# Optimization experiments

Hardware: AMD Instinct MI355X
Metric: run time of the kernel (lower is better)

Reference implementation:

```python
import jax, jax.numpy as jnp
import numpy as np

N = 2_097_152
TABLE = 32768  # hash table size (power of 2 -> mod == & 32767)
FEAT = 16
H = 64


def setup_inputs() -> dict:
    key = jax.random.key(0)
    k = jax.random.split(key, 9)
    pos = jax.random.normal(k[0], (N, 3), dtype=jnp.float32)
    normal = jax.random.normal(k[1], (N, 3), dtype=jnp.float32)
    emb = jax.random.normal(k[2], (TABLE, FEAT), dtype=jnp.float32) * 0.05
    W1 = jax.random.normal(k[3], (FEAT + 3, H), dtype=jnp.float32) * 0.1
    b1 = jnp.zeros((H,), jnp.float32)
    W2 = jax.random.normal(k[4], (H, H), dtype=jnp.float32) * 0.1
    b2 = jnp.zeros((H,), jnp.float32)
    W3 = jax.random.normal(k[5], (H, 3), dtype=jnp.float32) * 0.1
    b3 = jnp.zeros((3,), jnp.float32)
    return {"pos": pos, "normal": normal, "emb": emb,
            "W1": W1, "b1": b1, "W2": W2, "b2": b2, "W3": W3, "b3": b3}


def _hash_idx(pos):
    # torch .long() truncates toward zero; astype(int32) does the same.
    # Products only matter mod 2^15, so int32 wraparound is safe.
    s = (pos * 8.0).astype(jnp.int32)
    h = (s[:, 0] * np.int32(73856093)) ^ (s[:, 1] * np.int32(19349663)) ^ (s[:, 2] * np.int32(83492791))
    return h & np.int32(TABLE - 1)  # floor-mod by 2^15 == bitwise AND


def reference(pos, normal, emb, W1, b1, W2, b2, W3, b3):
    idx = _hash_idx(pos)                    # [N] int32
    feat = emb[idx]                         # [N,16] gather
    x = jnp.concatenate([feat, normal], axis=-1)  # [N,19]
    h1 = jax.nn.relu(x @ W1 + b1)           # [N,64]
    h2 = jax.nn.relu(h1 @ W2 + b2)          # [N,64]
    return jax.nn.sigmoid(h2 @ W3 + b3)     # [N,3]
```

## Files before the change

kernel.cpp:

```cpp
#include <hip/hip_runtime.h>
#include <cstdint>


typedef short  bf16x8 __attribute__((ext_vector_type(8)));
typedef float  f32x4  __attribute__((ext_vector_type(4)));

#define MFMA16(A, B, C) __builtin_amdgcn_mfma_f32_16x16x32_bf16((A), (B), (C), 0, 0, 0)

__device__ inline int pk(float a, float b) {
    int d;
    __asm__("v_cvt_pk_bf16_f32 %0, %1, %2" : "=v"(d) : "v"(a), "v"(b));
    return d;
}
__device__ inline uint32_t f2b_u(float f) {
    union { float f; uint32_t u; } x; x.f = f;
    return (x.u + 0x7FFFu + ((x.u >> 16) & 1u)) >> 16;
}
__device__ inline short f2b(float f) { return (short)f2b_u(f); }

__device__ inline void pl32_swap(int& a, int& b) {
    __asm__ volatile("v_permlane32_swap_b32 %0, %1" : "+v"(a), "+v"(b));
}
__device__ inline void pl16_swap(int& a, int& b) {
    __asm__ volatile("v_permlane16_swap_b32 %0, %1" : "+v"(a), "+v"(b));
}

__device__ inline void cfence() { __asm__ volatile("" ::: "memory"); }

__device__ inline float sigmoid_fast(float x) {
    float e = __expf(-x);
    return __builtin_amdgcn_rcpf(1.0f + e);
}

__device__ inline void cd_to_frag(const f32x4 acc[4], int4& lo, int4& hi) {
    int P0 = pk(fmaxf(acc[0][0],0.f), fmaxf(acc[0][1],0.f));
    int P1 = pk(fmaxf(acc[0][2],0.f), fmaxf(acc[0][3],0.f));
    int P2 = pk(fmaxf(acc[1][0],0.f), fmaxf(acc[1][1],0.f));
    int P3 = pk(fmaxf(acc[1][2],0.f), fmaxf(acc[1][3],0.f));
    int P4 = pk(fmaxf(acc[2][0],0.f), fmaxf(acc[2][1],0.f));
    int P5 = pk(fmaxf(acc[2][2],0.f), fmaxf(acc[2][3],0.f));
    int P6 = pk(fmaxf(acc[3][0],0.f), fmaxf(acc[3][1],0.f));
    int P7 = pk(fmaxf(acc[3][2],0.f), fmaxf(acc[3][3],0.f));
    pl32_swap(P0, P2); pl16_swap(P0, P2);
    pl32_swap(P1, P3); pl16_swap(P1, P3);
    pl32_swap(P4, P6); pl16_swap(P4, P6);
    pl32_swap(P5, P7); pl16_swap(P5, P7);
    lo = make_int4(P0, P1, P2, P3);
    hi = make_int4(P4, P5, P6, P7);
}

__device__ inline bf16x8 as_frag(int4 v) {
    bf16x8 f; __builtin_memcpy(&f, &v, sizeof(f)); return f;
}

#define XS 40

__global__ __launch_bounds__(256, 4) void nrad_mfma_kernel(
    const float* __restrict__ pos, const float* __restrict__ nrm,
    const float* __restrict__ emb,
    const float* __restrict__ W1, const float* __restrict__ b1,
    const float* __restrict__ W2, const float* __restrict__ b2,
    const float* __restrict__ W3, const float* __restrict__ b3,
    float* __restrict__ out, int ntiles)
{
    __shared__ alignas(16) char arena[20480];
    short* w1t = (short*)arena;
    short* w2t = (short*)(arena + 4096);
    short* w3t = (short*)(arena + 12288);
    float* b2s = (float*)(arena + 12672);
    float* b3s = (float*)(arena + 12928);

    const int tid  = threadIdx.x;
    const int wave = tid >> 6;
    const int lane = tid & 63;
    const int q    = lane >> 4;
    const int nn   = lane & 15;

    for (int e = tid; e < 64 * 32; e += 256) {
        int n = e >> 5, k = e & 31;
        float v = (k < 19) ? W1[k * 64 + n] : (k == 19 ? b1[n] : 0.0f);
        w1t[n * 32 + k] = f2b(v);
    }
    for (int e = tid; e < 4096; e += 256) {
        int k = e >> 6, n = e & 63;
        w2t[n * 64 + k] = f2b(W2[e]);
    }
    for (int e = tid; e < 192; e += 256) {
        int k = e / 3, c = e - k * 3;
        w3t[c * 64 + k] = f2b(W3[e]);
    }
    for (int e = tid; e < 64; e += 256) b2s[e] = b2[e];
    if (tid < 4) b3s[tid] = (tid < 3) ? b3[tid] : 0.0f;
    __syncthreads();

    bf16x8 w1f[4], w2f[4][2], w3f[2];
    #pragma unroll
    for (int t = 0; t < 4; ++t)
        w1f[t] = *(const bf16x8*)(w1t + (t * 16 + nn) * 32 + q * 8);
    #pragma unroll
    for (int t = 0; t < 4; ++t)
        #pragma unroll
        for (int ks = 0; ks < 2; ++ks)
            w2f[t][ks] = *(const bf16x8*)(w2t + (t * 16 + nn) * 64 + ks * 32 + q * 8);
    {
        int c3 = (nn < 3) ? nn : 0;
        w3f[0] = *(const bf16x8*)(w3t + c3 * 64 + q * 8);
        w3f[1] = *(const bf16x8*)(w3t + c3 * 64 + 32 + q * 8);
    }
    f32x4 b2rv[4];
    #pragma unroll
    for (int t = 0; t < 4; ++t)
        b2rv[t] = *(const f32x4*)(b2s + t * 16 + q * 4);
    const float b3r = (nn < 3) ? b3s[nn] : 0.0f;
    __syncthreads();

    short* xw = (short*)(arena + wave * 5120);

    const int xro  = nn * XS + q * 8;
    const int oofs = q * 12 + nn;

    const int wave_gid = blockIdx.x * 4 + wave;
    const int nwaves   = gridDim.x * 4;
    const float4* emb4 = (const float4*)emb;

    for (int tile = wave_gid; tile < ntiles; tile += nwaves) {
        const int base = tile * 64;
        const int i    = base + lane;

        const float* pp = pos + 3 * i;
        const float* np = nrm + 3 * i;
        float p0 = pp[0], p1 = pp[1], p2 = pp[2];
        float n0 = np[0], n1 = np[1], n2 = np[2];
        int s0 = (int)(p0 * 8.0f), s1 = (int)(p1 * 8.0f), s2 = (int)(p2 * 8.0f);
        uint32_t h = ((uint32_t)s0 * 73856093u) ^ ((uint32_t)s1 * 19349663u) ^
                     ((uint32_t)s2 * 83492791u);
        uint32_t idx = h & 32767u;
        float4 f0 = emb4[idx*4+0], f1 = emb4[idx*4+1];
        float4 f2 = emb4[idx*4+2], f3 = emb4[idx*4+3];

        int4 A = make_int4(pk(f0.x, f0.y), pk(f0.z, f0.w), pk(f1.x, f1.y), pk(f1.z, f1.w));
        int4 B = make_int4(pk(f2.x, f2.y), pk(f2.z, f2.w), pk(f3.x, f3.y), pk(f3.z, f3.w));
        int4 C = make_int4(pk(n0, n1), pk(n2, 1.0f), 0, 0);
        int4 D = make_int4(0, 0, 0, 0);
        int4* xr = (int4*)(xw + lane * XS);
        xr[0] = A; xr[1] = B; xr[2] = C; xr[3] = D;
        cfence();

        const float* ob = out + (size_t)base * 3;

        #pragma unroll
        for (int sub = 0; sub < 4; ++sub) {
            bf16x8 xf = *(const bf16x8*)(xw + sub * 16 * XS + xro);
            f32x4 acc1[4];
            #pragma unroll
            for (int t = 0; t < 4; ++t) {
                f32x4 z = {0.0f, 0.0f, 0.0f, 0.0f};
                acc1[t] = MFMA16(w1f[t], xf, z);
            }

            int4 h1lo, h1hi;
            cd_to_frag(acc1, h1lo, h1hi);
            bf16x8 h1f0 = as_frag(h1lo), h1f1 = as_frag(h1hi);

            f32x4 acc2[4];
            #pragma unroll
            for (int t = 0; t < 4; ++t) {
                f32x4 c2 = MFMA16(w2f[t][0], h1f0, b2rv[t]);
                acc2[t]  = MFMA16(w2f[t][1], h1f1, c2);
            }

            int4 h2lo, h2hi;
            cd_to_frag(acc2, h2lo, h2hi);
            bf16x8 h2f0 = as_frag(h2lo), h2f1 = as_frag(h2hi);

            f32x4 cb = {b3r, b3r, b3r, b3r};
            f32x4 c3a = MFMA16(h2f0, w3f[0], cb);
            f32x4 acc3 = MFMA16(h2f1, w3f[1], c3a);

            float o0 = sigmoid_fast(acc3[0]);
            float o1 = sigmoid_fast(acc3[1]);
            float o2 = sigmoid_fast(acc3[2]);
            float o3 = sigmoid_fast(acc3[3]);
            if (nn < 3) {
                float* o = (float*)(ob + sub * 48 + oofs);
                o[0] = o0; o[3] = o1; o[6] = o2; o[9] = o3;
            }
        }
        cfence();
    }
}

extern "C" void kernel_launch(void* const* d_in, const int* in_sizes, int n_in,
                              void* d_out, int out_size, void* d_ws, size_t ws_size,
                              hipStream_t stream) {
    const float* pos = (const float*)d_in[0];
    const float* nrm = (const float*)d_in[1];
    const float* emb = (const float*)d_in[2];
    const float* W1  = (const float*)d_in[3];
    const float* b1  = (const float*)d_in[4];
    const float* W2  = (const float*)d_in[5];
    const float* b2  = (const float*)d_in[6];
    const float* W3  = (const float*)d_in[7];
    const float* b3  = (const float*)d_in[8];
    float* out = (float*)d_out;

    int n = in_sizes[0] / 3;
    int ntiles = n / 64;
    int grid = 2048;
    nrad_mfma_kernel<<<grid, 256, 0, stream>>>(pos, nrm, emb, W1, b1, W2, b2,
                                               W3, b3, out, ntiles);
}
```

Before: 156.1 us.

## Prepack MLP weights in a setup kernel and interleave two MFMA sub-tiles

```diff
diff --git a/kernel.cpp b/kernel.cpp
--- a/kernel.cpp
+++ b/kernel.cpp
@@ -12,11 +12,6 @@
     __asm__("v_cvt_pk_bf16_f32 %0, %1, %2" : "=v"(d) : "v"(a), "v"(b));
     return d;
 }
-__device__ inline uint32_t f2b_u(float f) {
-    union { float f; uint32_t u; } x; x.f = f;
-    return (x.u + 0x7FFFu + ((x.u >> 16) & 1u)) >> 16;
-}
-__device__ inline short f2b(float f) { return (short)f2b_u(f); }
 
 __device__ inline void pl32_swap(int& a, int& b) {
     __asm__ volatile("v_permlane32_swap_b32 %0, %1" : "+v"(a), "+v"(b));
@@ -55,20 +50,68 @@
 
 #define XS 40
 
-__global__ __launch_bounds__(256, 4) void nrad_mfma_kernel(
+__global__ __launch_bounds__(256) void nrad_setup_kernel(
+    const float* __restrict__ W1, const float* __restrict__ b1,
+    const float* __restrict__ W2, const float* __restrict__ W3,
+    float* __restrict__ ws)
+{
+    const int tid  = threadIdx.x;
+    const int wv   = tid >> 6;
+    const int lane = tid & 63;
+    const int q    = lane >> 4;
+    const int nn   = lane & 15;
+    int4* w1o = (int4*)ws;
+    int4* w2o = (int4*)ws + 256;
+    int4* w3o = (int4*)ws + 768;
+
+    if (wv == 0) {
+        for (int t = 0; t < 4; ++t) {
+            int n = t * 16 + nn;
+            float v[8];
+            #pragma unroll
+            for (int j = 0; j < 8; ++j) {
+                int k = q * 8 + j;
+                v[j] = (k < 19) ? W1[k * 64 + n] : (k == 19 ? b1[n] : 0.0f);
+            }
+            w1o[t * 64 + lane] = make_int4(pk(v[0],v[1]), pk(v[2],v[3]),
+                                           pk(v[4],v[5]), pk(v[6],v[7]));
+        }
+    } else if (wv == 3) {
+        for (int h = 0; h < 2; ++h) {
+            float v[8];
+            #pragma unroll
+            for (int j = 0; j < 8; ++j) {
+                int k = h * 32 + q * 8 + j;
+                v[j] = (nn < 3) ? W3[k * 3 + nn] : 0.0f;
+            }
+            w3o[h * 64 + lane] = make_int4(pk(v[0],v[1]), pk(v[2],v[3]),
+                                           pk(v[4],v[5]), pk(v[6],v[7]));
+        }
+    } else {
+        for (int tt = 0; tt < 2; ++tt) {
+            int t = (wv - 1) * 2 + tt;
+            int n = t * 16 + nn;
+            for (int ks = 0; ks < 2; ++ks) {
+                float v[8];
+                #pragma unroll
+                for (int j = 0; j < 8; ++j) {
+                    int k = ks * 32 + q * 8 + j;
+                    v[j] = W2[k * 64 + n];
+                }
+                w2o[(t * 2 + ks) * 64 + lane] = make_int4(pk(v[0],v[1]), pk(v[2],v[3]),
+                                                          pk(v[4],v[5]), pk(v[6],v[7]));
+            }
+        }
+    }
+}
+
+__global__ __launch_bounds__(256, 3) void nrad_mfma_kernel(
     const float* __restrict__ pos, const float* __restrict__ nrm,
     const float* __restrict__ emb,
-    const float* __restrict__ W1, const float* __restrict__ b1,
-    const float* __restrict__ W2, const float* __restrict__ b2,
-    const float* __restrict__ W3, const float* __restrict__ b3,
-    float* __restrict__ out, int ntiles)
+    const float* __restrict__ b2, const float* __restrict__ b3,
+    const float* __restrict__ ws, float* __restrict__ out, int ntiles)
 {
-    __shared__ alignas(16) char arena[20480];
-    short* w1t = (short*)arena;
-    short* w2t = (short*)(arena + 4096);
-    short* w3t = (short*)(arena + 12288);
-    float* b2s = (float*)(arena + 12672);
-    float* b3s = (float*)(arena + 12928);
+    __shared__ alignas(16) short xbuf[4][64 * XS];
 
     const int tid  = threadIdx.x;
     const int wave = tid >> 6;
@@ -76,46 +119,23 @@
     const int q    = lane >> 4;
     const int nn   = lane & 15;
 
-    for (int e = tid; e < 64 * 32; e += 256) {
-        int n = e >> 5, k = e & 31;
-        float v = (k < 19) ? W1[k * 64 + n] : (k == 19 ? b1[n] : 0.0f);
-        w1t[n * 32 + k] = f2b(v);
-    }
-    for (int e = tid; e < 4096; e += 256) {
-        int k = e >> 6, n = e & 63;
-        w2t[n * 64 + k] = f2b(W2[e]);
-    }
-    for (int e = tid; e < 192; e += 256) {
-        int k = e / 3, c = e - k * 3;
-        w3t[c * 64 + k] = f2b(W3[e]);
-    }
-    for (int e = tid; e < 64; e += 256) b2s[e] = b2[e];
-    if (tid < 4) b3s[tid] = (tid < 3) ? b3[tid] : 0.0f;
-    __syncthreads();
-
+    const int4* wsf = (const int4*)ws;
     bf16x8 w1f[4], w2f[4][2], w3f[2];
     #pragma unroll
-    for (int t = 0; t < 4; ++t)
-        w1f[t] = *(const bf16x8*)(w1t + (t * 16 + nn) * 32 + q * 8);
+    for (int t = 0; t < 4; ++t) w1f[t] = as_frag(wsf[t * 64 + lane]);
     #pragma unroll
     for (int t = 0; t < 4; ++t)
         #pragma unroll
         for (int ks = 0; ks < 2; ++ks)
-            w2f[t][ks] = *(const bf16x8*)(w2t + (t * 16 + nn) * 64 + ks * 32 + q * 8);
-    {
-        int c3 = (nn < 3) ? nn : 0;
-        w3f[0] = *(const bf16x8*)(w3t + c3 * 64 + q * 8);
-        w3f[1] = *(const bf16x8*)(w3t + c3 * 64 + 32 + q * 8);
-    }
+            w2f[t][ks] = as_frag(wsf[256 + (t * 2 + ks) * 64 + lane]);
+    w3f[0] = as_frag(wsf[768 + lane]);
+    w3f[1] = as_frag(wsf[832 + lane]);
     f32x4 b2rv[4];
     #pragma unroll
-    for (int t = 0; t < 4; ++t)
-        b2rv[t] = *(const f32x4*)(b2s + t * 16 + q * 4);
-    const float b3r = (nn < 3) ? b3s[nn] : 0.0f;
-    __syncthreads();
-
-    short* xw = (short*)(arena + wave * 5120);
-
+    for (int t = 0; t < 4; ++t) b2rv[t] = *(const f32x4*)(b2 + t * 16 + q * 4);
+    const float b3r = (nn < 3) ? b3[nn] : 0.0f;
+
+    short* xw = &xbuf[wave][0];
     const int xro  = nn * XS + q * 8;
     const int oofs = q * 12 + nn;
 
@@ -147,43 +167,55 @@
         cfence();
 
         const float* ob = out + (size_t)base * 3;
+        const f32x4 z = {0.0f, 0.0f, 0.0f, 0.0f};
 
         #pragma unroll
-        for (int sub = 0; sub < 4; ++sub) {
-            bf16x8 xf = *(const bf16x8*)(xw + sub * 16 * XS + xro);
-            f32x4 acc1[4];
+        for (int sp = 0; sp < 2; ++sp) {
+            bf16x8 xfA = *(const bf16x8*)(xw + (2*sp)     * 16 * XS + xro);
+            bf16x8 xfB = *(const bf16x8*)(xw + (2*sp + 1) * 16 * XS + xro);
+
+            f32x4 a1A[4], a1B[4];
+            #pragma unroll
+            for (int t = 0; t < 4; ++t) a1A[t] = MFMA16(w1f[t], xfA, z);
+            #pragma unroll
+            for (int t = 0; t < 4; ++t) a1B[t] = MFMA16(w1f[t], xfB, z);
+
+            int4 lA, hA, lB, hB;
+            cd_to_frag(a1A, lA, hA);
+            cd_to_frag(a1B, lB, hB);
+            bf16x8 h1A0 = as_frag(lA), h1A1 = as_frag(hA);
+            bf16x8 h1B0 = as_frag(lB), h1B1 = as_frag(hB);
+
+            f32x4 a2A[4], a2B[4];
             #pragma unroll
             for (int t = 0; t < 4; ++t) {
-                f32x4 z = {0.0f, 0.0f, 0.0f, 0.0f};
-                acc1[t] = MFMA16(w1f[t], xf, z);
-            }
-
-            int4 h1lo, h1hi;
-            cd_to_frag(acc1, h1lo, h1hi);
-            bf16x8 h1f0 = as_frag(h1lo), h1f1 = as_frag(h1hi);
-
-            f32x4 acc2[4];
+                f32x4 c = MFMA16(w2f[t][0], h1A0, b2rv[t]);
+                a2A[t]  = MFMA16(w2f[t][1], h1A1, c);
+            }
             #pragma unroll
             for (int t = 0; t < 4; ++t) {
-                f32x4 c2 = MFMA16(w2f[t][0], h1f0, b2rv[t]);
-                acc2[t]  = MFMA16(w2f[t][1], h1f1, c2);
-            }
-
-            int4 h2lo, h2hi;
-            cd_to_frag(acc2, h2lo, h2hi);
-            bf16x8 h2f0 = as_frag(h2lo), h2f1 = as_frag(h2hi);
+                f32x4 c = MFMA16(w2f[t][0], h1B0, b2rv[t]);
+                a2B[t]  = MFMA16(w2f[t][1], h1B1, c);
+            }
+
+            cd_to_frag(a2A, lA, hA);
+            cd_to_frag(a2B, lB, hB);
+            bf16x8 h2A0 = as_frag(lA), h2A1 = as_frag(hA);
+            bf16x8 h2B0 = as_frag(lB), h2B1 = as_frag(hB);
 
             f32x4 cb = {b3r, b3r, b3r, b3r};
-            f32x4 c3a = MFMA16(h2f0, w3f[0], cb);
-            f32x4 acc3 = MFMA16(h2f1, w3f[1], c3a);
-
-            float o0 = sigmoid_fast(acc3[0]);
-            float o1 = sigmoid_fast(acc3[1]);
-            float o2 = sigmoid_fast(acc3[2]);
-            float o3 = sigmoid_fast(acc3[3]);
+            f32x4 acc3A = MFMA16(h2A1, w3f[1], MFMA16(h2A0, w3f[0], cb));
+            f32x4 acc3B = MFMA16(h2B1, w3f[1], MFMA16(h2B0, w3f[0], cb));
+
+            float oA0 = sigmoid_fast(acc3A[0]), oA1 = sigmoid_fast(acc3A[1]);
+            float oA2 = sigmoid_fast(acc3A[2]), oA3 = sigmoid_fast(acc3A[3]);
+            float oB0 = sigmoid_fast(acc3B[0]), oB1 = sigmoid_fast(acc3B[1]);
+            float oB2 = sigmoid_fast(acc3B[2]), oB3 = sigmoid_fast(acc3B[3]);
             if (nn < 3) {
-                float* o = (float*)(ob + sub * 48 + oofs);
-                o[0] = o0; o[3] = o1; o[6] = o2; o[9] = o3;
+                float* oa = (float*)(ob + (2*sp)     * 48 + oofs);
+                float* obp= (float*)(ob + (2*sp + 1) * 48 + oofs);
+                oa[0] = oA0; oa[3] = oA1; oa[6] = oA2; oa[9] = oA3;
+                obp[0] = oB0; obp[3] = oB1; obp[6] = oB2; obp[9] = oB3;
             }
         }
         cfence();
@@ -203,10 +235,12 @@
     const float* W3  = (const float*)d_in[7];
     const float* b3  = (const float*)d_in[8];
     float* out = (float*)d_out;
+    float* ws  = (float*)d_ws;
 
     int n = in_sizes[0] / 3;
     int ntiles = n / 64;
-    int grid = 2048;
-    nrad_mfma_kernel<<<grid, 256, 0, stream>>>(pos, nrm, emb, W1, b1, W2, b2,
-                                               W3, b3, out, ntiles);
-}
+
+    nrad_setup_kernel<<<1, 256, 0, stream>>>(W1, b1, W2, W3, ws);
+    nrad_mfma_kernel<<<2048, 256, 0, stream>>>(pos, nrm, emb, b2, b3, ws,
+                                               out, ntiles);
+}
```

Result: faster. 148.9 us (-4.6%).
